# Kernel tuning notes

Hardware: AMD Instinct MI355X
Metric: run time of the kernel (lower is better)

Reference implementation:

```python
import jax, jax.numpy as jnp
import numpy as np

ALPHA = 10.0 / 100.0  # dt / tau

def setup_inputs() -> dict:
    key = jax.random.key(0)
    ks = jax.random.split(key, 5)
    seq_len, batch, input_size, hidden_size = 512, 64, 256, 1024
    x = jax.random.normal(ks[0], (seq_len, batch, input_size), dtype=jnp.float32)
    h0 = jnp.zeros((batch, hidden_size), dtype=jnp.float32)
    Wx = jax.random.normal(ks[1], (hidden_size, input_size), dtype=jnp.float32) / np.sqrt(input_size)
    bx = jax.random.normal(ks[2], (hidden_size,), dtype=jnp.float32) * 0.01
    Wh = jax.random.normal(ks[3], (hidden_size, hidden_size), dtype=jnp.float32) / np.sqrt(hidden_size)
    bh = jax.random.normal(ks[4], (hidden_size,), dtype=jnp.float32) * 0.01
    return {"x": x, "h0": h0, "Wx": Wx, "bx": bx, "Wh": Wh, "bh": bh}

def reference(x, h0, Wx, bx, Wh, bh):
    # Precompute input projection for all timesteps in one GEMM: [S,B,H]
    xproj = jnp.einsum('sbi,hi->sbh', x, Wx) + bx

    def step(h, xp_t):
        h_new = jax.nn.relu(xp_t + h @ Wh.T + bh)
        h = h * (1.0 - ALPHA) + h_new * ALPHA
        return h, h

    h_final, output = jax.lax.scan(step, h0, xproj)
    return output, h_final
```

## Files before the change

kernel.cpp:

```cpp
#include <hip/hip_runtime.h>
#include <stdint.h>

#define S_LEN 512
#define BATCH 64
#define INSZ  256
#define HID   1024
#define BH    (BATCH*HID)
#define NPIPE 8
#define ROWSP 8
#define NCG   32
#define SMEM_BYTES (131072 + 16384)
#define WS_PLANES_OFF 4096
#define PLANE_STRIDE (ROWSP*HID)
#define WS_NEEDED (WS_PLANES_OFF + NPIPE*2*2*PLANE_STRIDE*2)
#define FLAG_IDX(p, c) ((p)*128 + ((c)>>3)*32 + ((c)&7))

typedef __attribute__((ext_vector_type(8))) short short8;
typedef __attribute__((ext_vector_type(4))) short short4v;
typedef __attribute__((ext_vector_type(4))) float f32x4;
typedef __attribute__((ext_vector_type(4))) float f4;
typedef __attribute__((ext_vector_type(4))) unsigned int u32x4;

__device__ __forceinline__ uint32_t bf16_rne(float x) {
  uint32_t u = __float_as_uint(x);
  return (u + 0x7fffu + ((u >> 16) & 1u)) >> 16;
}
__device__ __forceinline__ void cvt_pair(float v, short& h, short& l) {
  uint32_t hb = bf16_rne(v);
  float hf = __uint_as_float(hb << 16);
  uint32_t lb = bf16_rne(v - hf);
  h = (short)hb; l = (short)lb;
}
__device__ __forceinline__ void cvt8(f4 a0, f4 a1, short8& hi, short8& lo) {
  #pragma unroll
  for (int e = 0; e < 4; ++e) { short h, l; cvt_pair(a0[e], h, l); hi[e] = h; lo[e] = l; }
  #pragma unroll
  for (int e = 0; e < 4; ++e) { short h, l; cvt_pair(a1[e], h, l); hi[4+e] = h; lo[4+e] = l; }
}

#define MFMA(A, B, C) __builtin_amdgcn_mfma_f32_16x16x32_bf16((A), (B), (C), 0, 0, 0)
#define WAIT_VM0() do { asm volatile("s_waitcnt vmcnt(0)" ::: "memory"); \
                        __builtin_amdgcn_sched_barrier(0); } while (0)

__device__ __forceinline__ void llc_load_f4(f4& d, const float* p) {
  asm volatile("global_load_dwordx4 %0, %1, off sc0 sc1" : "=v"(d) : "v"(p) : "memory");
}
__device__ __forceinline__ void llc_load_s8(short8& d, const uint16_t* p) {
  asm volatile("global_load_dwordx4 %0, %1, off sc0 sc1" : "=v"(d) : "v"(p) : "memory");
}
__device__ __forceinline__ void llc_store_f4(float* p, f4 v) {
  asm volatile("global_store_dwordx4 %0, %1, off sc0 sc1" :: "v"(p), "v"(v) : "memory");
}
__device__ __forceinline__ void llc_store_s4(uint16_t* p, short4v v) {
  asm volatile("global_store_dwordx2 %0, %1, off sc0 sc1" :: "v"(p), "v"(v) : "memory");
}
__device__ __forceinline__ void llc_store_u16(uint16_t* p, uint32_t v) {
  asm volatile("global_store_short %0, %1, off sc0 sc1" :: "v"(p), "v"(v) : "memory");
}
__device__ __forceinline__ void llc_store_u32(uint32_t* p, uint32_t v) {
  asm volatile("global_store_dword %0, %1, off sc0 sc1" :: "v"(p), "v"(v) : "memory");
}
__device__ __forceinline__ uint32_t poll_min8(const uint32_t* p) {
  u32x4 a, b;
  asm volatile("global_load_dwordx4 %0, %2, off sc0 sc1\n\t"
               "global_load_dwordx4 %1, %2, off offset:16 sc0 sc1\n\t"
               "s_waitcnt vmcnt(0)"
               : "=&v"(a), "=&v"(b) : "v"(p) : "memory");
  uint32_t m = a.x;
  m = a.y < m ? a.y : m;  m = a.z < m ? a.z : m;  m = a.w < m ? a.w : m;
  m = b.x < m ? b.x : m;  m = b.y < m ? b.y : m;  m = b.z < m ? b.z : m;
  m = b.w < m ? b.w : m;
  return m;
}

__global__ void ctrnn_init(uint32_t* ws) {
  const int i = threadIdx.x;
  ws[i] = 0; ws[i + 256] = 0; ws[i + 512] = 0; ws[i + 768] = 0;
}

template<bool SPLIT>
__global__ __launch_bounds__(256, 1)
void ctrnn_main(const float* __restrict__ x,  const float* __restrict__ h0,
                const float* __restrict__ Wx, const float* __restrict__ bx,
                const float* __restrict__ Wh, const float* __restrict__ bh,
                float* __restrict__ out, uint32_t* ws)
{
  extern __shared__ char smem_raw[];
  short* pHi = (short*)smem_raw;
  short* pLo = pHi + 32768;
  float* red = (float*)(smem_raw + 131072);

  const int tid  = threadIdx.x;
  const int wg   = blockIdx.x;
  const int lane = tid & 63;
  const int wave = tid >> 6;
  const int l15  = lane & 15;
  const int kg   = lane >> 4;

  for (int tt = 0; tt < 2; ++tt) {
    const int t = wg * 2 + tt;
    if (tt) __syncthreads();
    {
      const float* xt = x + (size_t)t * (BATCH * INSZ);
      #pragma unroll
      for (int it = 0; it < 16; ++it) {
        const int flat4 = (it * 256 + tid) * 4;
        const int b = flat4 >> 8;
        const int k = flat4 & 255;
        f4 v = *(const f4*)(xt + b * INSZ + k);
        short4v hv, lv;
        #pragma unroll
        for (int e = 0; e < 4; ++e) { short h, l; cvt_pair(v[e], h, l); hv[e] = h; lv[e] = l; }
        const int si = b * 256 + (k ^ ((b & 7) << 3));
        *(short4v*)(pHi + si) = hv;
        *(short4v*)(pLo + si) = lv;
      }
    }
    __syncthreads();
    for (int ntl = 0; ntl < 16; ++ntl) {
      const int nt = wave * 16 + ntl;
      const int nn = nt * 16 + l15;
      f32x4 acc0 = {0,0,0,0}, acc1 = {0,0,0,0}, acc2 = {0,0,0,0}, acc3 = {0,0,0,0};
      #pragma unroll
      for (int kt = 0; kt < 8; ++kt) {
        const int k = kt * 32 + kg * 8;
        const float* wp = Wx + (size_t)nn * INSZ + k;
        short8 bhi8, blo8;
        cvt8(*(const f4*)wp, *(const f4*)(wp + 4), bhi8, blo8);
        const int swz = (l15 & 7) << 3;
        short8 a0h = *(const short8*)(pHi + (     l15) * 256 + (k ^ swz));
        short8 a0l = *(const short8*)(pLo + (     l15) * 256 + (k ^ swz));
        short8 a1h = *(const short8*)(pHi + (16 + l15) * 256 + (k ^ swz));
        short8 a1l = *(const short8*)(pLo + (16 + l15) * 256 + (k ^ swz));
        short8 a2h = *(const short8*)(pHi + (32 + l15) * 256 + (k ^ swz));
        short8 a2l = *(const short8*)(pLo + (32 + l15) * 256 + (k ^ swz));
        short8 a3h = *(const short8*)(pHi + (48 + l15) * 256 + (k ^ swz));
        short8 a3l = *(const short8*)(pLo + (48 + l15) * 256 + (k ^ swz));
        acc0 = MFMA(a0h, bhi8, acc0);
        acc1 = MFMA(a1h, bhi8, acc1);
        acc2 = MFMA(a2h, bhi8, acc2);
        acc3 = MFMA(a3h, bhi8, acc3);
        acc0 = MFMA(a0l, bhi8, acc0);
        acc1 = MFMA(a1l, bhi8, acc1);
        acc2 = MFMA(a2l, bhi8, acc2);
        acc3 = MFMA(a3l, bhi8, acc3);
        acc0 = MFMA(a0h, blo8, acc0);
        acc1 = MFMA(a1h, blo8, acc1);
        acc2 = MFMA(a2h, blo8, acc2);
        acc3 = MFMA(a3h, blo8, acc3);
      }
      const float bxn = bx[nn];
      float* op = out + (size_t)t * BH;
      #pragma unroll
      for (int i = 0; i < 4; ++i) {
        const int b0 = kg * 4 + i;
        op[(size_t)(     b0) * HID + nn] = acc0[i] + bxn;
        op[(size_t)(16 + b0) * HID + nn] = acc1[i] + bxn;
        op[(size_t)(32 + b0) * HID + nn] = acc2[i] + bxn;
        op[(size_t)(48 + b0) * HID + nn] = acc3[i] + bxn;
      }
    }
  }

  __syncthreads();
  const int pipe = wg >> 5;
  const int cg   = wg & 31;
  const int rbase = pipe * ROWSP;
  #pragma unroll
  for (int it = 0; it < 32; ++it) {
    const int flat4 = (it * 256 + tid) * 4;
    const int r = flat4 >> 10;
    const int k = flat4 & 1023;
    f4 w = *(const f4*)(Wh + (size_t)(cg * 32 + r) * HID + k);
    short4v hv, lv;
    #pragma unroll
    for (int e = 0; e < 4; ++e) { short h, l; cvt_pair(w[e], h, l); hv[e] = h; lv[e] = l; }
    const int si = r * 1024 + (k ^ ((r & 7) << 3));
    *(short4v*)(pHi + si) = hv;
    *(short4v*)(pLo + si) = lv;
  }

  uint16_t* planes = (uint16_t*)((char*)ws + WS_PLANES_OFF);

  if (SPLIT) {
    const int r = tid >> 5, c = tid & 31;
    const float v = h0[(size_t)(rbase + r) * HID + cg * 32 + c];
    short h, l; cvt_pair(v, h, l);
    uint16_t* bH = planes + ((pipe * 2 + 1) * 2 + 0) * PLANE_STRIDE + r * HID + cg * 32 + c;
    llc_store_u16(bH, (uint32_t)(uint16_t)h);
    llc_store_u16(bH + PLANE_STRIDE, (uint32_t)(uint16_t)l);
  }

  const int er = lane >> 3, ejc = lane & 7;
  f4 hp = {0,0,0,0}, bhv = {0,0,0,0};
  if (wave == 0) {
    hp  = *(const f4*)(h0 + (size_t)(rbase + er) * HID + cg * 32 + ejc * 4);
    bhv = *(const f4*)(bh + cg * 32 + ejc * 4);
  }

  asm volatile("s_waitcnt vmcnt(0)" ::: "memory");
  __syncthreads();

  uint32_t* gbar = ws + 8;
  if (tid == 0) {
    __hip_atomic_fetch_add(gbar, 1u, __ATOMIC_RELEASE, __HIP_MEMORY_SCOPE_AGENT);
    int spins = 0;
    while (__hip_atomic_load(gbar, __ATOMIC_RELAXED, __HIP_MEMORY_SCOPE_AGENT) < 256u) {
      __builtin_amdgcn_s_sleep(8);
      if (++spins > (1 << 20)) break;
    }
  }
  __syncthreads();
  __builtin_amdgcn_fence(__ATOMIC_ACQUIRE, "agent");

  uint32_t* flags = ws;
  uint32_t* myflag = flags + FLAG_IDX(pipe, cg);
  const uint32_t* pollbase = flags + pipe * 128 + wave * 32;

  for (int t = 0; t < S_LEN; ++t) {
    float* op = out + (size_t)t * BH;
    const int buf_r = (t + 1) & 1, buf_w = t & 1;

    f4 xv = {0,0,0,0};
    if (wave == 0)
      xv = *(const f4*)(op + (size_t)(rbase + er) * HID + cg * 32 + ejc * 4);

    if (t > 0 && lane == 0) {
      int spins = 0;
      while (poll_min8(pollbase) < (uint32_t)t) {
        if (++spins > 64) __builtin_amdgcn_s_sleep(1);
        if (spins > (1 << 20)) break;
      }
    }

    short8 ah[8], al[8];
    #pragma unroll
    for (int kk = 0; kk < 8; ++kk) { ah[kk] = (short8)0; al[kk] = (short8)0; }
    if (SPLIT) {
      if (l15 < 8) {
        const uint16_t* pH = planes + ((pipe * 2 + buf_r) * 2 + 0) * PLANE_STRIDE
                             + l15 * HID + wave * 256 + kg * 8;
        const uint16_t* pL = pH + PLANE_STRIDE;
        #pragma unroll
        for (int kk = 0; kk < 8; ++kk) {
          llc_load_s8(ah[kk], pH + kk * 32);
          llc_load_s8(al[kk], pL + kk * 32);
        }
      }
      WAIT_VM0();
    } else {
      f4 a[8][2];
      #pragma unroll
      for (int kk = 0; kk < 8; ++kk) { a[kk][0] = (f4){0,0,0,0}; a[kk][1] = (f4){0,0,0,0}; }
      if (l15 < 8) {
        const float* hrow = (t ? (op - BH) : h0)
                            + (size_t)(rbase + l15) * HID + wave * 256 + kg * 8;
        #pragma unroll
        for (int kk = 0; kk < 8; ++kk) {
          llc_load_f4(a[kk][0], hrow + kk * 32);
          llc_load_f4(a[kk][1], hrow + kk * 32 + 4);
        }
      }
      WAIT_VM0();
      #pragma unroll
      for (int kk = 0; kk < 8; ++kk) cvt8(a[kk][0], a[kk][1], ah[kk], al[kk]);
    }

    f32x4 acc0 = {0,0,0,0}, acc1 = {0,0,0,0};
    #pragma unroll
    for (int kk = 0; kk < 8; ++kk) {
      const int k = wave * 256 + kk * 32 + kg * 8;
      const int si = (k ^ ((l15 & 7) << 3));
      short8 b0h = *(const short8*)(pHi + l15 * 1024 + si);
      short8 b0l = *(const short8*)(pLo + l15 * 1024 + si);
      short8 b1h = *(const short8*)(pHi + (16 + l15) * 1024 + si);
      short8 b1l = *(const short8*)(pLo + (16 + l15) * 1024 + si);
      acc0 = MFMA(ah[kk], b0h, acc0);
      acc0 = MFMA(al[kk], b0h, acc0);
      acc0 = MFMA(ah[kk], b0l, acc0);
      acc1 = MFMA(ah[kk], b1h, acc1);
      acc1 = MFMA(al[kk], b1h, acc1);
      acc1 = MFMA(ah[kk], b1l, acc1);
    }

    float* rb = red + buf_w * 2048;
    *(f32x4*)(rb + wave * 512 + lane * 4) = acc0;
    *(f32x4*)(rb + wave * 512 + 256 + lane * 4) = acc1;
    __syncthreads();

    if (wave == 0) {
      f4 s;
      #pragma unroll
      for (int e = 0; e < 4; ++e) {
        const int tc = ejc * 4 + e;
        const int idx = (tc >> 4) * 256 + (((er >> 2) * 16 + (tc & 15)) * 4) + (er & 3);
        float a0 = rb[idx] + rb[512 + idx];
        float a1 = rb[1024 + idx] + rb[1536 + idx];
        s[e] = a0 + a1;
      }
      f4 hn;
      #pragma unroll
      for (int e = 0; e < 4; ++e) hn[e] = fmaxf(xv[e] + s[e] + bhv[e], 0.0f);
      #pragma unroll
      for (int e = 0; e < 4; ++e) hp[e] = 0.9f * hp[e] + 0.1f * hn[e];

      if (SPLIT) {
        short4v h4, l4;
        #pragma unroll
        for (int e = 0; e < 4; ++e) { short h, l; cvt_pair(hp[e], h, l); h4[e] = h; l4[e] = l; }
        uint16_t* bH = planes + ((pipe * 2 + buf_w) * 2 + 0) * PLANE_STRIDE
                       + er * HID + cg * 32 + ejc * 4;
        llc_store_s4(bH, h4);
        llc_store_s4(bH + PLANE_STRIDE, l4);
        asm volatile("s_waitcnt vmcnt(0)" ::: "memory");
        if (lane == 0) llc_store_u32(myflag, (uint32_t)(t + 1));
        *(f4*)(op + (size_t)(rbase + er) * HID + cg * 32 + ejc * 4) = hp;
        if (t == S_LEN - 1)
          *(f4*)(out + (size_t)S_LEN * BH + (size_t)(rbase + er) * HID + cg * 32 + ejc * 4) = hp;
      } else {
        llc_store_f4(op + (size_t)(rbase + er) * HID + cg * 32 + ejc * 4, hp);
        asm volatile("s_waitcnt vmcnt(0)" ::: "memory");
        if (lane == 0) llc_store_u32(myflag, (uint32_t)(t + 1));
        if (t == S_LEN - 1)
          llc_store_f4(out + (size_t)S_LEN * BH + (size_t)(rbase + er) * HID + cg * 32 + ejc * 4, hp);
      }
    }
  }
}

extern "C" void kernel_launch(void* const* d_in, const int* in_sizes, int n_in,
                              void* d_out, int out_size, void* d_ws, size_t ws_size,
                              hipStream_t stream) {
  (void)in_sizes; (void)n_in; (void)out_size;
  const float* x  = (const float*)d_in[0];
  const float* h0 = (const float*)d_in[1];
  const float* Wx = (const float*)d_in[2];
  const float* bx = (const float*)d_in[3];
  const float* Wh = (const float*)d_in[4];
  const float* bh = (const float*)d_in[5];
  float* out = (float*)d_out;
  uint32_t* ws = (uint32_t*)d_ws;

  ctrnn_init<<<1, 256, 0, stream>>>(ws);
  if (ws_size >= (size_t)WS_NEEDED) {
    hipFuncSetAttribute((const void*)ctrnn_main<true>,
                        hipFuncAttributeMaxDynamicSharedMemorySize, SMEM_BYTES);
    ctrnn_main<true><<<256, 256, SMEM_BYTES, stream>>>(x, h0, Wx, bx, Wh, bh, out, ws);
  } else {
    hipFuncSetAttribute((const void*)ctrnn_main<false>,
                        hipFuncAttributeMaxDynamicSharedMemorySize, SMEM_BYTES);
    ctrnn_main<false><<<256, 256, SMEM_BYTES, stream>>>(x, h0, Wx, bx, Wh, bh, out, ws);
  }
}
```

Measured before the change: 2.349 ms.

## Embed step-parity tag bits in bf16 planes to overlap loads with flag polling

Encodes a two-bit timestep tag into the low mantissa bits of selected bf16 hi/lo values written to the shared hidden-state planes. Readers now issue the plane loads before the flag poll and then validate the tag bits, reloading until every value carries the expected tag. The writer also drops the waitcnt between the data stores and the flag store. The aim is to hide cross-block synchronization latency on the serial recurrence by overlapping data fetches with the flag poll. In exchange it loses one mantissa bit of precision on half the elements and adds retry loops. It also relies on data validation rather than strict store ordering for correctness.

```diff
diff --git a/kernel.cpp b/kernel.cpp
--- a/kernel.cpp
+++ b/kernel.cpp
@@ -185,10 +185,15 @@
   if (SPLIT) {
     const int r = tid >> 5, c = tid & 31;
     const float v = h0[(size_t)(rbase + r) * HID + cg * 32 + c];
-    short h, l; cvt_pair(v, h, l);
+    uint32_t hb = bf16_rne(v);
+    const bool vb = ((c & 3) == 1) || ((c & 3) == 3);
+    if (vb) hb &= ~1u;
+    float hf = __uint_as_float(hb << 16);
+    uint32_t lb = bf16_rne(v - hf);
+    if (vb) lb &= ~1u;
     uint16_t* bH = planes + ((pipe * 2 + 1) * 2 + 0) * PLANE_STRIDE + r * HID + cg * 32 + c;
-    llc_store_u16(bH, (uint32_t)(uint16_t)h);
-    llc_store_u16(bH + PLANE_STRIDE, (uint32_t)(uint16_t)l);
+    llc_store_u16(bH, hb & 0xffffu);
+    llc_store_u16(bH + PLANE_STRIDE, lb & 0xffffu);
   }
 
   const int er = lane >> 3, ejc = lane & 7;
@@ -225,30 +230,68 @@
     if (wave == 0)
       xv = *(const f4*)(op + (size_t)(rbase + er) * HID + cg * 32 + ejc * 4);
 
-    if (t > 0 && lane == 0) {
-      int spins = 0;
-      while (poll_min8(pollbase) < (uint32_t)t) {
-        if (++spins > 64) __builtin_amdgcn_s_sleep(1);
-        if (spins > (1 << 20)) break;
-      }
-    }
-
     short8 ah[8], al[8];
     #pragma unroll
     for (int kk = 0; kk < 8; ++kk) { ah[kk] = (short8)0; al[kk] = (short8)0; }
+
     if (SPLIT) {
+      const uint16_t* pH = planes + ((pipe * 2 + buf_r) * 2 + 0) * PLANE_STRIDE
+                           + l15 * HID + wave * 256 + kg * 8;
+      const uint16_t* pL = pH + PLANE_STRIDE;
       if (l15 < 8) {
-        const uint16_t* pH = planes + ((pipe * 2 + buf_r) * 2 + 0) * PLANE_STRIDE
-                             + l15 * HID + wave * 256 + kg * 8;
-        const uint16_t* pL = pH + PLANE_STRIDE;
         #pragma unroll
         for (int kk = 0; kk < 8; ++kk) {
           llc_load_s8(ah[kk], pH + kk * 32);
           llc_load_s8(al[kk], pL + kk * 32);
         }
       }
+      if (t > 0 && lane == 0) {
+        int spins = 0;
+        while (poll_min8(pollbase) < (uint32_t)t) {
+          if (++spins > 64) __builtin_amdgcn_s_sleep(1);
+          if (spins > (1 << 20)) break;
+        }
+      }
       WAIT_VM0();
+      const uint32_t vb0 = (uint32_t)(t & 1);
+      const uint32_t vb1 = (uint32_t)((t >> 1) & 1);
+      int attempts = 0;
+      for (;;) {
+        uint32_t bad = 0;
+        if (l15 < 8) {
+          #pragma unroll
+          for (int kk = 0; kk < 8; ++kk) {
+            bad |= ((uint32_t)ah[kk][1] ^ vb0) & 1u;
+            bad |= ((uint32_t)ah[kk][3] ^ vb1) & 1u;
+            bad |= ((uint32_t)ah[kk][5] ^ vb0) & 1u;
+            bad |= ((uint32_t)ah[kk][7] ^ vb1) & 1u;
+            bad |= ((uint32_t)al[kk][1] ^ vb0) & 1u;
+            bad |= ((uint32_t)al[kk][3] ^ vb1) & 1u;
+            bad |= ((uint32_t)al[kk][5] ^ vb0) & 1u;
+            bad |= ((uint32_t)al[kk][7] ^ vb1) & 1u;
+          }
+        }
+        if (__all(bad == 0)) break;
+        if (++attempts > (1 << 16)) break;
+        if ((attempts & 3) == 0) __builtin_amdgcn_s_sleep(1);
+        asm volatile("" : "+v"(pH), "+v"(pL));
+        if (l15 < 8) {
+          #pragma unroll
+          for (int kk = 0; kk < 8; ++kk) {
+            llc_load_s8(ah[kk], pH + kk * 32);
+            llc_load_s8(al[kk], pL + kk * 32);
+          }
+        }
+        WAIT_VM0();
+      }
     } else {
+      if (t > 0 && lane == 0) {
+        int spins = 0;
+        while (poll_min8(pollbase) < (uint32_t)t) {
+          if (++spins > 64) __builtin_amdgcn_s_sleep(1);
+          if (spins > (1 << 20)) break;
+        }
+      }
       f4 a[8][2];
       #pragma unroll
       for (int kk = 0; kk < 8; ++kk) { a[kk][0] = (f4){0,0,0,0}; a[kk][1] = (f4){0,0,0,0}; }
@@ -305,14 +348,25 @@
       for (int e = 0; e < 4; ++e) hp[e] = 0.9f * hp[e] + 0.1f * hn[e];
 
       if (SPLIT) {
+        const uint32_t wb0 = (uint32_t)((t + 1) & 1);
+        const uint32_t wb1 = (uint32_t)(((t + 1) >> 1) & 1);
         short4v h4, l4;
         #pragma unroll
-        for (int e = 0; e < 4; ++e) { short h, l; cvt_pair(hp[e], h, l); h4[e] = h; l4[e] = l; }
+        for (int e = 0; e < 4; ++e) {
+          float v = hp[e];
+          uint32_t hb = bf16_rne(v);
+          if (e == 1) hb = (hb & ~1u) | wb0;
+          if (e == 3) hb = (hb & ~1u) | wb1;
+          float hf = __uint_as_float(hb << 16);
+          uint32_t lb = bf16_rne(v - hf);
+          if (e == 1) lb = (lb & ~1u) | wb0;
+          if (e == 3) lb = (lb & ~1u) | wb1;
+          h4[e] = (short)hb; l4[e] = (short)lb;
+        }
         uint16_t* bH = planes + ((pipe * 2 + buf_w) * 2 + 0) * PLANE_STRIDE
                        + er * HID + cg * 32 + ejc * 4;
         llc_store_s4(bH, h4);
         llc_store_s4(bH + PLANE_STRIDE, l4);
-        asm volatile("s_waitcnt vmcnt(0)" ::: "memory");
         if (lane == 0) llc_store_u32(myflag, (uint32_t)(t + 1));
         *(f4*)(op + (size_t)(rbase + er) * HID + cg * 32 + ejc * 4) = hp;
         if (t == S_LEN - 1)
```

Measured after the change: 2.999 ms. 27.7% more time.
